# Optimization experiments

Measured on AMD Instinct MI355X. Metric: run time of the kernel, lower is better.

## Reference

```python
import jax, jax.numpy as jnp
import numpy as np

ROUTINGS = 3
NUM_CAPSULE = 32
DIM_CAPSULE = 64
K_EPSILON = 1e-7  # keras K.epsilon()


def squash(x, axis=-1):
    s = jnp.sum(jnp.square(x), axis=axis, keepdims=True) + K_EPSILON
    scale = jnp.sqrt(s) / (0.5 + s)
    return scale * x


def setup_inputs() -> dict:
    key = jax.random.key(0)
    k1, k2 = jax.random.split(key)
    B, N_in, D_in = 32, 1024, 512
    u = jax.random.normal(k1, (B, N_in, D_in), dtype=jnp.float32)
    # glorot_uniform for capsule_kernel (conv1d width-1 kernel == dense matrix)
    fan_out = NUM_CAPSULE * DIM_CAPSULE
    limit = float(np.sqrt(6.0 / (D_in + fan_out)))
    W = jax.random.uniform(k2, (D_in, fan_out), jnp.float32, -limit, limit)
    return {"u": u, "W": W}


def reference(u, W):
    B, N_in, _ = u.shape
    # K.conv1d with width-1 kernel == matmul, then reshape
    u_hat = (u @ W).reshape(B, N_in, NUM_CAPSULE, DIM_CAPSULE)
    u_hat = jnp.transpose(u_hat, (0, 2, 1, 3))  # [B, N_out, N_in, D]
    b = jnp.zeros(u_hat.shape[:3], u_hat.dtype)  # [B, N_out, N_in]
    vj = None
    for i in range(ROUTINGS):
        Wv = jax.nn.softmax(b, axis=1)  # softmax over output capsules (axis=1)
        vj = jnp.einsum('bon,bond->bod', Wv, u_hat)  # batch_dot(Wv,u_hat,[2,2])
        if i < ROUTINGS - 1:
            # K.l2_normalize(vj) with default axis=None -> global L2 norm
            norm = jnp.sqrt(jnp.maximum(jnp.sum(jnp.square(vj)), 1e-12))
            vjn = vj / norm
            b = jnp.einsum('bod,bond->bon', vjn, u_hat)  # batch_dot(vj,u_hat,[2,3])
    return squash(vj)
```

## Files before the change

kernel.cpp:

```cpp
#include <hip/hip_runtime.h>
#include <hip/hip_bf16.h>


constexpr int B = 32, N = 1024, K = 512, O = 32, D = 64, F = 2048;
constexpr int NT = 32;
constexpr int ST = 72;

typedef __attribute__((ext_vector_type(8))) short bf16x8;
typedef __attribute__((ext_vector_type(4))) float f32x4;

__device__ inline unsigned int pk_hi(float x, float y) {
  union { __hip_bfloat162 h; unsigned int u; } c;
  c.h = __float22bfloat162_rn(float2{x, y});
  return c.u;
}
__device__ inline unsigned short bf16_1(float x) {
  return (unsigned short)(pk_hi(x, 0.f) & 0xffffu);
}
__device__ inline void split2(float x, unsigned short& h, unsigned short& l) {
  h = bf16_1(x);
  l = bf16_1(x - __uint_as_float((unsigned int)h << 16));
}
__device__ inline int swz(int r) { return ((r >> 3) & 7) << 3; }

__device__ inline void stage_hi(unsigned short* hi, int r, int c4, float4 v) {
  int c = c4 ^ swz(r);
  uint2 p;
  p.x = pk_hi(v.x, v.y);
  p.y = pk_hi(v.z, v.w);
  *(uint2*)&hi[r * ST + c] = p;
}
__device__ inline void stage_hilo(unsigned short* hi, unsigned short* lo, int r,
                                  int c4, float4 v) {
  int c = c4 ^ swz(r);
  uint2 ph, pl;
  ph.x = pk_hi(v.x, v.y);
  ph.y = pk_hi(v.z, v.w);
  pl.x = pk_hi(v.x - __uint_as_float(ph.x << 16),
               v.y - __uint_as_float(ph.x & 0xffff0000u));
  pl.y = pk_hi(v.z - __uint_as_float(ph.y << 16),
               v.w - __uint_as_float(ph.y & 0xffff0000u));
  *(uint2*)&hi[r * ST + c] = ph;
  *(uint2*)&lo[r * ST + c] = pl;
}
__device__ inline bf16x8 frag_row(const unsigned short* p, int r, int k0) {
  return *(const bf16x8*)&p[r * ST + (k0 ^ swz(r))];
}
__device__ inline bf16x8 frag_col(const unsigned short* p, int c, int n0) {
  bf16x8 f;
#pragma unroll
  for (int j = 0; j < 8; j++) {
    int n = n0 + j;
    f[j] = (short)p[n * ST + (c ^ swz(n))];
  }
  return f;
}

__global__ __launch_bounds__(256) void k_colsum(const float* __restrict__ u,
                                                float* __restrict__ cs) {
  int b = blockIdx.x, n0 = blockIdx.y * 32;
  int kq = (threadIdx.x & 127) * 4, ng = threadIdx.x >> 7;
  const float* ub = u + ((size_t)b * N + n0 + ng * 16) * K + kq;
  float4 a = {0.f, 0.f, 0.f, 0.f};
#pragma unroll
  for (int r = 0; r < 16; r++) {
    float4 v = *(const float4*)&ub[(size_t)r * K];
    a.x += v.x; a.y += v.y; a.z += v.z; a.w += v.w;
  }
  __shared__ float4 red[128];
  if (ng) red[threadIdx.x & 127] = a;
  __syncthreads();
  if (!ng) {
    float4 o = red[threadIdx.x];
    atomicAdd(&cs[b * K + kq + 0], (a.x + o.x) * (1.f / 32.f));
    atomicAdd(&cs[b * K + kq + 1], (a.y + o.y) * (1.f / 32.f));
    atomicAdd(&cs[b * K + kq + 2], (a.z + o.z) * (1.f / 32.f));
    atomicAdd(&cs[b * K + kq + 3], (a.w + o.w) * (1.f / 32.f));
  }
}

__global__ __launch_bounds__(512) void k_vjt(const float* __restrict__ Sp,
                                             const float* __restrict__ colsum,
                                             const float* __restrict__ W,
                                             float* __restrict__ sumsq, int slot,
                                             float* __restrict__ t) {
  __shared__ __align__(16) float s_s[K];
  __shared__ float red[7][D];
  __shared__ __align__(16) float vs[D];
  int bo = blockIdx.x, b = bo >> 5, o = bo & 31;
  int d = threadIdx.x & 63, ks = threadIdx.x >> 6;
  if (slot == 0) {
    for (int i = threadIdx.x; i < K; i += 512) s_s[i] = colsum[(size_t)b * K + i];
  } else {
    const float* base = Sp + ((size_t)b * NT * O + o) * K;
    int i = threadIdx.x;
    float a = 0.f;
#pragma unroll
    for (int nt = 0; nt < NT; nt++) a += base[(size_t)nt * O * K + i];
    s_s[i] = a;
  }
  __syncthreads();
  float acc = 0.f;
  const float* Wc = W + (size_t)o * D + d;
  for (int k = ks * 64; k < ks * 64 + 64; k += 4) {
    acc += s_s[k] * Wc[(size_t)k * F] + s_s[k + 1] * Wc[(size_t)(k + 1) * F] +
           s_s[k + 2] * Wc[(size_t)(k + 2) * F] + s_s[k + 3] * Wc[(size_t)(k + 3) * F];
  }
  if (ks) red[ks - 1][d] = acc;
  __syncthreads();
  if (ks == 0) {
#pragma unroll
    for (int j = 0; j < 7; j++) acc += red[j][d];
    vs[d] = acc;
    float ss = acc * acc;
#pragma unroll
    for (int m = 32; m >= 1; m >>= 1) ss += __shfl_xor(ss, m, 64);
    if (d == 0) atomicAdd(&sumsq[slot], ss);
  }
  __syncthreads();
  {
    int wave = threadIdx.x >> 6, lane = threadIdx.x & 63;
    int rr = lane >> 3, dc = lane & 7;
    float4 va = *(const float4*)&vs[dc * 8];
    float4 vb = *(const float4*)&vs[dc * 8 + 4];
#pragma unroll
    for (int i = 0; i < 8; i++) {
      int kk = wave * 64 + i * 8 + rr;
      const float* Wr = W + (size_t)kk * F + o * 64 + dc * 8;
      float4 wa = *(const float4*)Wr;
      float4 wb = *(const float4*)(Wr + 4);
      float p = wa.x * va.x + wa.y * va.y + wa.z * va.z + wa.w * va.w +
                wb.x * vb.x + wb.y * vb.y + wb.z * vb.z + wb.w * vb.w;
      p += __shfl_xor(p, 1, 64);
      p += __shfl_xor(p, 2, 64);
      p += __shfl_xor(p, 4, 64);
      if (dc == 0) t[(size_t)bo * K + kk] = p;
    }
  }
}

__global__ __launch_bounds__(512) void k_out(const float* __restrict__ Sp,
                                             const float* __restrict__ W,
                                             float* __restrict__ out) {
  __shared__ __align__(16) float s_s[K];
  __shared__ float red[7][D];
  int bo = blockIdx.x, b = bo >> 5, o = bo & 31;
  int d = threadIdx.x & 63, ks = threadIdx.x >> 6;
  {
    const float* base = Sp + ((size_t)b * NT * O + o) * K;
    int i = threadIdx.x;
    float a = 0.f;
#pragma unroll
    for (int nt = 0; nt < NT; nt++) a += base[(size_t)nt * O * K + i];
    s_s[i] = a;
  }
  __syncthreads();
  float acc = 0.f;
  const float* Wc = W + (size_t)o * D + d;
  for (int k = ks * 64; k < ks * 64 + 64; k += 4) {
    acc += s_s[k] * Wc[(size_t)k * F] + s_s[k + 1] * Wc[(size_t)(k + 1) * F] +
           s_s[k + 2] * Wc[(size_t)(k + 2) * F] + s_s[k + 3] * Wc[(size_t)(k + 3) * F];
  }
  if (ks) red[ks - 1][d] = acc;
  __syncthreads();
  if (ks == 0) {
#pragma unroll
    for (int j = 0; j < 7; j++) acc += red[j][d];
    float ss = acc * acc;
#pragma unroll
    for (int m = 32; m >= 1; m >>= 1) ss += __shfl_xor(ss, m, 64);
    float s = ss + 1e-7f;
    out[(size_t)bo * D + d] = (sqrtf(s) / (0.5f + s)) * acc;
  }
}

__global__ __launch_bounds__(256, 4) void k_route(const float* __restrict__ t,
                                                  const float* __restrict__ u,
                                                  const float* __restrict__ sumsq,
                                                  int slot, float* __restrict__ Sp) {
  __shared__ unsigned short u_hi[32 * ST];
  __shared__ unsigned short t_hi[32 * ST], t_lo[32 * ST];
  __shared__ float wv[32 * 36];
  __shared__ float psum[8 * 36];
  __shared__ float mbuf[36];
  unsigned short* wvh = t_hi;
  unsigned short* wvl = t_lo;

  const int b = blockIdx.x, n0 = blockIdx.y * 32;
  const int tid = threadIdx.x, lane = tid & 63, wave = tid >> 6;
  const int m = lane & 15, oct = lane >> 4;
  const float* ub = u + ((size_t)b * N + n0) * K;
  const float* tb = t + (size_t)b * O * K;
  const float nrm_inv = rsqrtf(fmaxf(sumsq[slot], 1e-12f));

  const int mo = wave & 1, nt = wave >> 1;
  f32x4 accb = {0.f, 0.f, 0.f, 0.f};
  for (int kc = 0; kc < K; kc += 64) {
    __syncthreads();
#pragma unroll
    for (int h = 0; h < 2; h++) {
      int i = tid + h * 256;
      int r = i >> 4, c4 = (i & 15) * 4;
      stage_hilo(t_hi, t_lo, r, c4, *(const float4*)&tb[(size_t)r * K + kc + c4]);
      stage_hi(u_hi, r, c4, *(const float4*)&ub[(size_t)r * K + kc + c4]);
    }
    __syncthreads();
#pragma unroll
    for (int ks = 0; ks < 64; ks += 32) {
      bf16x8 ah = frag_row(t_hi, mo * 16 + m, ks + oct * 8);
      bf16x8 al = frag_row(t_lo, mo * 16 + m, ks + oct * 8);
      bf16x8 bh = frag_row(u_hi, nt * 16 + m, ks + oct * 8);
      accb = __builtin_amdgcn_mfma_f32_16x16x32_bf16(ah, bh, accb, 0, 0, 0);
      accb = __builtin_amdgcn_mfma_f32_16x16x32_bf16(al, bh, accb, 0, 0, 0);
    }
  }
  __syncthreads();
#pragma unroll
  for (int r = 0; r < 4; r++)
    wv[(mo * 16 + oct * 4 + r) * 36 + nt * 16 + m] = accb[r] * nrm_inv;
  __syncthreads();

  {
    int n = tid & 31, g = tid >> 5;
    float m4 = -1e30f;
#pragma unroll
    for (int j = 0; j < 4; j++) m4 = fmaxf(m4, wv[(g * 4 + j) * 36 + n]);
    psum[g * 36 + n] = m4;
    __syncthreads();
    if (tid < 32) {
      float mx = psum[tid];
#pragma unroll
      for (int gg = 1; gg < 8; gg++) mx = fmaxf(mx, psum[gg * 36 + tid]);
      mbuf[tid] = mx;
    }
    __syncthreads();
    float mx = mbuf[n];
    float s4 = 0.f;
#pragma unroll
    for (int j = 0; j < 4; j++) {
      float e = __expf(wv[(g * 4 + j) * 36 + n] - mx);
      wv[(g * 4 + j) * 36 + n] = e;
      s4 += e;
    }
    psum[g * 36 + n] = s4;
    __syncthreads();
    if (tid < 32) {
      float s = 0.f;
#pragma unroll
      for (int gg = 0; gg < 8; gg++) s += psum[gg * 36 + tid];
      mbuf[tid] = 1.f / s;
    }
    __syncthreads();
    float inv = mbuf[n];
#pragma unroll
    for (int j = 0; j < 4; j++) {
      unsigned short h, l;
      split2(wv[(g * 4 + j) * 36 + n] * inv, h, l);
      wvh[(g * 4 + j) * ST + n] = h;
      wvl[(g * 4 + j) * ST + n] = l;
    }
  }
  __syncthreads();

  const int mo2 = wave & 1, kp = wave >> 1;
  const int o0 = mo2 * 16;
  bf16x8 a_h = *(const bf16x8*)&wvh[(o0 + m) * ST + oct * 8];
  bf16x8 a_l = *(const bf16x8*)&wvl[(o0 + m) * ST + oct * 8];
  float* Sb = Sp + ((size_t)b * NT + blockIdx.y) * O * K;
  for (int kc = 0; kc < K; kc += 64) {
    __syncthreads();
#pragma unroll
    for (int h = 0; h < 2; h++) {
      int i = tid + h * 256;
      int r = i >> 4, c4 = (i & 15) * 4;
      stage_hi(u_hi, r, c4, *(const float4*)&ub[(size_t)r * K + kc + c4]);
    }
    __syncthreads();
#pragma unroll
    for (int kt = kp * 2; kt < kp * 2 + 2; kt++) {
      int c = kt * 16 + m;
      bf16x8 bh = frag_col(u_hi, c, oct * 8);
      f32x4 acs = {0.f, 0.f, 0.f, 0.f};
      acs = __builtin_amdgcn_mfma_f32_16x16x32_bf16(a_h, bh, acs, 0, 0, 0);
      acs = __builtin_amdgcn_mfma_f32_16x16x32_bf16(a_l, bh, acs, 0, 0, 0);
#pragma unroll
      for (int r = 0; r < 4; r++)
        Sb[(size_t)(o0 + oct * 4 + r) * K + kc + c] = acs[r];
    }
  }
}

extern "C" void kernel_launch(void* const* d_in, const int* in_sizes, int n_in,
                              void* d_out, int out_size, void* d_ws, size_t ws_size,
                              hipStream_t stream) {
  const float* u = (const float*)d_in[0];
  const float* W = (const float*)d_in[1];
  float* out = (float*)d_out;

  float* ws = (float*)d_ws;
  float* Sp = ws;
  float* t = Sp + (size_t)B * NT * O * K;
  float* colsum = t + (size_t)B * O * K;
  float* sumsq = colsum + (size_t)B * K;

  hipMemsetAsync(colsum, 0, ((size_t)B * K + 16) * sizeof(float), stream);

  k_colsum<<<dim3(B, 32), 256, 0, stream>>>(u, colsum);
  k_vjt<<<B * O, 512, 0, stream>>>(Sp, colsum, W, sumsq, 0, t);
  k_route<<<dim3(B, NT), 256, 0, stream>>>(t, u, sumsq, 0, Sp);
  k_vjt<<<B * O, 512, 0, stream>>>(Sp, colsum, W, sumsq, 1, t);
  k_route<<<dim3(B, NT), 256, 0, stream>>>(t, u, sumsq, 1, Sp);
  k_out<<<B * O, 512, 0, stream>>>(Sp, W, out);
}
```

Baseline: 215.3 us.

## Precompute bf16 copies of u (row and transposed) once and stream fragments directly

The colsum kernel becomes a prep kernel that also writes bf16 copies of u in both row-major and transposed layouts, and k_vjt writes t already split into bf16 hi/lo parts. k_route then loads MFMA fragments straight from global memory with no LDS staging, f32-to-bf16 conversion or per-chunk barriers, so u is read as 2-byte values in each routing pass instead of 4-byte floats. The cost is extra global writes of two bf16 copies of u (64 MB total) plus a transpose through LDS in the prep kernel, and fragment loads from the transposed copy are strided across rows.

```diff
diff --git a/kernel.cpp b/kernel.cpp
--- a/kernel.cpp
+++ b/kernel.cpp
@@ -4,7 +4,6 @@
 
 constexpr int B = 32, N = 1024, K = 512, O = 32, D = 64, F = 2048;
 constexpr int NT = 32;
-constexpr int ST = 72;
 
 typedef __attribute__((ext_vector_type(8))) short bf16x8;
 typedef __attribute__((ext_vector_type(4))) float f32x4;
@@ -21,69 +20,61 @@
   h = bf16_1(x);
   l = bf16_1(x - __uint_as_float((unsigned int)h << 16));
 }
-__device__ inline int swz(int r) { return ((r >> 3) & 7) << 3; }
-
-__device__ inline void stage_hi(unsigned short* hi, int r, int c4, float4 v) {
-  int c = c4 ^ swz(r);
-  uint2 p;
-  p.x = pk_hi(v.x, v.y);
-  p.y = pk_hi(v.z, v.w);
-  *(uint2*)&hi[r * ST + c] = p;
-}
-__device__ inline void stage_hilo(unsigned short* hi, unsigned short* lo, int r,
-                                  int c4, float4 v) {
-  int c = c4 ^ swz(r);
-  uint2 ph, pl;
-  ph.x = pk_hi(v.x, v.y);
-  ph.y = pk_hi(v.z, v.w);
-  pl.x = pk_hi(v.x - __uint_as_float(ph.x << 16),
-               v.y - __uint_as_float(ph.x & 0xffff0000u));
-  pl.y = pk_hi(v.z - __uint_as_float(ph.y << 16),
-               v.w - __uint_as_float(ph.y & 0xffff0000u));
-  *(uint2*)&hi[r * ST + c] = ph;
-  *(uint2*)&lo[r * ST + c] = pl;
-}
-__device__ inline bf16x8 frag_row(const unsigned short* p, int r, int k0) {
-  return *(const bf16x8*)&p[r * ST + (k0 ^ swz(r))];
-}
-__device__ inline bf16x8 frag_col(const unsigned short* p, int c, int n0) {
-  bf16x8 f;
-#pragma unroll
-  for (int j = 0; j < 8; j++) {
-    int n = n0 + j;
-    f[j] = (short)p[n * ST + (c ^ swz(n))];
-  }
-  return f;
-}
-
-__global__ __launch_bounds__(256) void k_colsum(const float* __restrict__ u,
-                                                float* __restrict__ cs) {
+
+__global__ __launch_bounds__(256) void k_prep(const float* __restrict__ u,
+                                              float* __restrict__ cs,
+                                              unsigned short* __restrict__ u_bf,
+                                              unsigned short* __restrict__ uT_bf) {
+  __shared__ unsigned short uTl[512 * 34];
+  __shared__ float4 red[128];
   int b = blockIdx.x, n0 = blockIdx.y * 32;
-  int kq = (threadIdx.x & 127) * 4, ng = threadIdx.x >> 7;
+  int tid = threadIdx.x;
+  int kq = (tid & 127) * 4, ng = tid >> 7;
   const float* ub = u + ((size_t)b * N + n0 + ng * 16) * K + kq;
   float4 a = {0.f, 0.f, 0.f, 0.f};
 #pragma unroll
-  for (int r = 0; r < 16; r++) {
-    float4 v = *(const float4*)&ub[(size_t)r * K];
+  for (int nn = 0; nn < 16; nn++) {
+    float4 v = *(const float4*)&ub[(size_t)nn * K];
     a.x += v.x; a.y += v.y; a.z += v.z; a.w += v.w;
-  }
-  __shared__ float4 red[128];
-  if (ng) red[threadIdx.x & 127] = a;
+    uint2 p;
+    p.x = pk_hi(v.x, v.y);
+    p.y = pk_hi(v.z, v.w);
+    int n = ng * 16 + nn;
+    *(uint2*)&u_bf[((size_t)b * N + n0 + n) * K + kq] = p;
+    uTl[(kq + 0) * 34 + n] = (unsigned short)(p.x & 0xffff);
+    uTl[(kq + 1) * 34 + n] = (unsigned short)(p.x >> 16);
+    uTl[(kq + 2) * 34 + n] = (unsigned short)(p.y & 0xffff);
+    uTl[(kq + 3) * 34 + n] = (unsigned short)(p.y >> 16);
+  }
+  if (ng) red[tid & 127] = a;
   __syncthreads();
   if (!ng) {
-    float4 o = red[threadIdx.x];
+    float4 o = red[tid];
     atomicAdd(&cs[b * K + kq + 0], (a.x + o.x) * (1.f / 32.f));
     atomicAdd(&cs[b * K + kq + 1], (a.y + o.y) * (1.f / 32.f));
     atomicAdd(&cs[b * K + kq + 2], (a.z + o.z) * (1.f / 32.f));
     atomicAdd(&cs[b * K + kq + 3], (a.w + o.w) * (1.f / 32.f));
   }
+  __syncthreads();
+#pragma unroll
+  for (int h = 0; h < 8; h++) {
+    int i = tid + h * 256;
+    int k = i >> 2, c = i & 3;
+    uint4 v;
+    v.x = *(const unsigned int*)&uTl[k * 34 + 8 * c + 0];
+    v.y = *(const unsigned int*)&uTl[k * 34 + 8 * c + 2];
+    v.z = *(const unsigned int*)&uTl[k * 34 + 8 * c + 4];
+    v.w = *(const unsigned int*)&uTl[k * 34 + 8 * c + 6];
+    *(uint4*)&uT_bf[((size_t)b * K + k) * N + n0 + 8 * c] = v;
+  }
 }
 
 __global__ __launch_bounds__(512) void k_vjt(const float* __restrict__ Sp,
                                              const float* __restrict__ colsum,
                                              const float* __restrict__ W,
                                              float* __restrict__ sumsq, int slot,
-                                             float* __restrict__ t) {
+                                             unsigned short* __restrict__ t_hi,
+                                             unsigned short* __restrict__ t_lo) {
   __shared__ __align__(16) float s_s[K];
   __shared__ float red[7][D];
   __shared__ __align__(16) float vs[D];
@@ -134,7 +125,12 @@
       p += __shfl_xor(p, 1, 64);
       p += __shfl_xor(p, 2, 64);
       p += __shfl_xor(p, 4, 64);
-      if (dc == 0) t[(size_t)bo * K + kk] = p;
+      if (dc == 0) {
+        unsigned short h, l;
+        split2(p, h, l);
+        t_hi[(size_t)bo * K + kk] = h;
+        t_lo[(size_t)bo * K + kk] = l;
+      }
     }
   }
 }
@@ -174,47 +170,36 @@
   }
 }
 
-__global__ __launch_bounds__(256, 4) void k_route(const float* __restrict__ t,
-                                                  const float* __restrict__ u,
-                                                  const float* __restrict__ sumsq,
-                                                  int slot, float* __restrict__ Sp) {
-  __shared__ unsigned short u_hi[32 * ST];
-  __shared__ unsigned short t_hi[32 * ST], t_lo[32 * ST];
+__global__ __launch_bounds__(256) void k_route(const unsigned short* __restrict__ t_hi,
+                                               const unsigned short* __restrict__ t_lo,
+                                               const unsigned short* __restrict__ u_bf,
+                                               const unsigned short* __restrict__ uT_bf,
+                                               const float* __restrict__ sumsq,
+                                               int slot, float* __restrict__ Sp) {
   __shared__ float wv[32 * 36];
   __shared__ float psum[8 * 36];
   __shared__ float mbuf[36];
-  unsigned short* wvh = t_hi;
-  unsigned short* wvl = t_lo;
+  __shared__ unsigned short wvh[32 * 40], wvl[32 * 40];
 
   const int b = blockIdx.x, n0 = blockIdx.y * 32;
   const int tid = threadIdx.x, lane = tid & 63, wave = tid >> 6;
   const int m = lane & 15, oct = lane >> 4;
-  const float* ub = u + ((size_t)b * N + n0) * K;
-  const float* tb = t + (size_t)b * O * K;
   const float nrm_inv = rsqrtf(fmaxf(sumsq[slot], 1e-12f));
 
   const int mo = wave & 1, nt = wave >> 1;
+  const unsigned short* th = t_hi + ((size_t)b * O + mo * 16 + m) * K;
+  const unsigned short* tl = t_lo + ((size_t)b * O + mo * 16 + m) * K;
+  const unsigned short* ubf = u_bf + ((size_t)b * N + n0 + nt * 16 + m) * K;
   f32x4 accb = {0.f, 0.f, 0.f, 0.f};
-  for (int kc = 0; kc < K; kc += 64) {
-    __syncthreads();
-#pragma unroll
-    for (int h = 0; h < 2; h++) {
-      int i = tid + h * 256;
-      int r = i >> 4, c4 = (i & 15) * 4;
-      stage_hilo(t_hi, t_lo, r, c4, *(const float4*)&tb[(size_t)r * K + kc + c4]);
-      stage_hi(u_hi, r, c4, *(const float4*)&ub[(size_t)r * K + kc + c4]);
-    }
-    __syncthreads();
-#pragma unroll
-    for (int ks = 0; ks < 64; ks += 32) {
-      bf16x8 ah = frag_row(t_hi, mo * 16 + m, ks + oct * 8);
-      bf16x8 al = frag_row(t_lo, mo * 16 + m, ks + oct * 8);
-      bf16x8 bh = frag_row(u_hi, nt * 16 + m, ks + oct * 8);
-      accb = __builtin_amdgcn_mfma_f32_16x16x32_bf16(ah, bh, accb, 0, 0, 0);
-      accb = __builtin_amdgcn_mfma_f32_16x16x32_bf16(al, bh, accb, 0, 0, 0);
-    }
-  }
-  __syncthreads();
+#pragma unroll 4
+  for (int kc = 0; kc < K; kc += 32) {
+    int k0 = kc + oct * 8;
+    bf16x8 ah = *(const bf16x8*)&th[k0];
+    bf16x8 al = *(const bf16x8*)&tl[k0];
+    bf16x8 bh = *(const bf16x8*)&ubf[k0];
+    accb = __builtin_amdgcn_mfma_f32_16x16x32_bf16(ah, bh, accb, 0, 0, 0);
+    accb = __builtin_amdgcn_mfma_f32_16x16x32_bf16(al, bh, accb, 0, 0, 0);
+  }
 #pragma unroll
   for (int r = 0; r < 4; r++)
     wv[(mo * 16 + oct * 4 + r) * 36 + nt * 16 + m] = accb[r] * nrm_inv;
@@ -256,37 +241,28 @@
     for (int j = 0; j < 4; j++) {
       unsigned short h, l;
       split2(wv[(g * 4 + j) * 36 + n] * inv, h, l);
-      wvh[(g * 4 + j) * ST + n] = h;
-      wvl[(g * 4 + j) * ST + n] = l;
+      wvh[(g * 4 + j) * 40 + n] = h;
+      wvl[(g * 4 + j) * 40 + n] = l;
     }
   }
   __syncthreads();
 
   const int mo2 = wave & 1, kp = wave >> 1;
   const int o0 = mo2 * 16;
-  bf16x8 a_h = *(const bf16x8*)&wvh[(o0 + m) * ST + oct * 8];
-  bf16x8 a_l = *(const bf16x8*)&wvl[(o0 + m) * ST + oct * 8];
+  bf16x8 a_h = *(const bf16x8*)&wvh[(o0 + m) * 40 + oct * 8];
+  bf16x8 a_l = *(const bf16x8*)&wvl[(o0 + m) * 40 + oct * 8];
+  const unsigned short* uTb = uT_bf + (size_t)b * K * N + n0;
   float* Sb = Sp + ((size_t)b * NT + blockIdx.y) * O * K;
-  for (int kc = 0; kc < K; kc += 64) {
-    __syncthreads();
-#pragma unroll
-    for (int h = 0; h < 2; h++) {
-      int i = tid + h * 256;
-      int r = i >> 4, c4 = (i & 15) * 4;
-      stage_hi(u_hi, r, c4, *(const float4*)&ub[(size_t)r * K + kc + c4]);
-    }
-    __syncthreads();
-#pragma unroll
-    for (int kt = kp * 2; kt < kp * 2 + 2; kt++) {
-      int c = kt * 16 + m;
-      bf16x8 bh = frag_col(u_hi, c, oct * 8);
-      f32x4 acs = {0.f, 0.f, 0.f, 0.f};
-      acs = __builtin_amdgcn_mfma_f32_16x16x32_bf16(a_h, bh, acs, 0, 0, 0);
-      acs = __builtin_amdgcn_mfma_f32_16x16x32_bf16(a_l, bh, acs, 0, 0, 0);
-#pragma unroll
-      for (int r = 0; r < 4; r++)
-        Sb[(size_t)(o0 + oct * 4 + r) * K + kc + c] = acs[r];
-    }
+#pragma unroll 4
+  for (int it = 0; it < 16; it++) {
+    int kcol = it * 32 + kp * 16 + m;
+    bf16x8 bh = *(const bf16x8*)&uTb[(size_t)kcol * N + oct * 8];
+    f32x4 acs = {0.f, 0.f, 0.f, 0.f};
+    acs = __builtin_amdgcn_mfma_f32_16x16x32_bf16(a_h, bh, acs, 0, 0, 0);
+    acs = __builtin_amdgcn_mfma_f32_16x16x32_bf16(a_l, bh, acs, 0, 0, 0);
+#pragma unroll
+    for (int r = 0; r < 4; r++)
+      Sb[(size_t)(o0 + oct * 4 + r) * K + kcol] = acs[r];
   }
 }
 
@@ -299,16 +275,19 @@
 
   float* ws = (float*)d_ws;
   float* Sp = ws;
-  float* t = Sp + (size_t)B * NT * O * K;
-  float* colsum = t + (size_t)B * O * K;
+  unsigned short* u_bf = (unsigned short*)(Sp + (size_t)B * NT * O * K);
+  unsigned short* uT_bf = u_bf + (size_t)B * N * K;
+  unsigned short* t_hi = uT_bf + (size_t)B * N * K;
+  unsigned short* t_lo = t_hi + (size_t)B * O * K;
+  float* colsum = (float*)(t_lo + (size_t)B * O * K);
   float* sumsq = colsum + (size_t)B * K;
 
   hipMemsetAsync(colsum, 0, ((size_t)B * K + 16) * sizeof(float), stream);
 
-  k_colsum<<<dim3(B, 32), 256, 0, stream>>>(u, colsum);
-  k_vjt<<<B * O, 512, 0, stream>>>(Sp, colsum, W, sumsq, 0, t);
-  k_route<<<dim3(B, NT), 256, 0, stream>>>(t, u, sumsq, 0, Sp);
-  k_vjt<<<B * O, 512, 0, stream>>>(Sp, colsum, W, sumsq, 1, t);
-  k_route<<<dim3(B, NT), 256, 0, stream>>>(t, u, sumsq, 1, Sp);
+  k_prep<<<dim3(B, N / 32), 256, 0, stream>>>(u, colsum, u_bf, uT_bf);
+  k_vjt<<<B * O, 512, 0, stream>>>(Sp, colsum, W, sumsq, 0, t_hi, t_lo);
+  k_route<<<dim3(B, NT), 256, 0, stream>>>(t_hi, t_lo, u_bf, uT_bf, sumsq, 0, Sp);
+  k_vjt<<<B * O, 512, 0, stream>>>(Sp, colsum, W, sumsq, 1, t_hi, t_lo);
+  k_route<<<dim3(B, NT), 256, 0, stream>>>(t_hi, t_lo, u_bf, uT_bf, sumsq, 1, Sp);
   k_out<<<B * O, 512, 0, stream>>>(Sp, W, out);
 }
```

New measurement: 252.8 us. 1.17x slower.
